# Kernel tuning notes

Measured on AMD Instinct MI355X. Metric: run time of the kernel, lower is better.

Reference implementation:

```python
import jax, jax.numpy as jnp
import numpy as np

MAX_AGENTS = 5
AGENT_DIM = 64
NUM_ACTIONS = 10
BATCH = 131072


def setup_inputs() -> dict:
    key = jax.random.key(0)
    ks = jax.random.split(key, 20)
    def lin(k, out_d, in_d):
        kw, kb = jax.random.split(k)
        W = jax.random.normal(kw, (out_d, in_d), jnp.float32) * (1.0 / np.sqrt(in_d))
        b = jax.random.normal(kb, (out_d,), jnp.float32) * 0.02
        return W, b
    x = jax.random.normal(ks[0], (BATCH, MAX_AGENTS * AGENT_DIM), jnp.float32)
    Wk, bk = lin(ks[1], 32, AGENT_DIM)
    Wq, bq = lin(ks[2], 32, AGENT_DIM)
    Wv, bv = lin(ks[3], 64, AGENT_DIM)
    Wr, br = lin(ks[4], 32, 32)
    Wp1, bp1 = lin(ks[5], 64, 64)
    Wp2, bp2 = lin(ks[6], MAX_AGENTS * NUM_ACTIONS, 64)
    Wh1, bh1 = lin(ks[7], 64, 64)
    Wh2, bh2 = lin(ks[8], 1, 64)
    return {"x": x, "Wk": Wk, "bk": bk, "Wq": Wq, "bq": bq, "Wv": Wv, "bv": bv,
            "Wr": Wr, "br": br, "Wp1": Wp1, "bp1": bp1, "Wp2": Wp2, "bp2": bp2,
            "Wh1": Wh1, "bh1": bh1, "Wh2": Wh2, "bh2": bh2}


def reference(x, Wk, bk, Wq, bq, Wv, bv, Wr, br, Wp1, bp1, Wp2, bp2, Wh1, bh1, Wh2, bh2):
    B = x.shape[0]
    agents = x.reshape(B, MAX_AGENTS, AGENT_DIM)  # [B, A, D]
    keys = agents @ Wk.T + bk      # [B, A, 32]
    queries = agents @ Wq.T + bq   # [B, A, 32]
    values = agents @ Wv.T + bv    # [B, A, 64]
    scale = 1.0 / np.sqrt(32.0)
    attn = jnp.einsum('bqd,bkd->bqk', queries, keys) * scale
    rq = queries @ Wr.T + br       # [B, A, 32]
    attn = attn + jnp.einsum('bqd,bkd->bqk', rq, rq) * scale
    attn = jax.nn.softmax(attn, axis=-1)
    context = jnp.einsum('bqk,bkd->bqd', attn, values)  # [B, A, 64]
    agent_mask = (jnp.abs(agents).sum(axis=-1, keepdims=True) > 0.01).astype(x.dtype)  # [B, A, 1]
    pooled = (context * agent_mask).sum(axis=1) / (agent_mask.sum(axis=1) + 1e-8)  # [B, 64]
    h = jax.nn.gelu(pooled @ Wp1.T + bp1, approximate=False)
    action_logits = (h @ Wp2.T + bp2).reshape(B, MAX_AGENTS, NUM_ACTIONS)
    hv = jax.nn.gelu(pooled @ Wh1.T + bh1, approximate=False)
    value = hv @ Wh2.T + bh2  # [B, 1]
    return action_logits, value
```

## Files before the change

kernel.cpp:

```cpp
#include <hip/hip_runtime.h>
#include <stdint.h>


typedef __attribute__((ext_vector_type(8))) short bf16x8;
typedef __attribute__((ext_vector_type(4))) float f32x4;

#define ESTR 168
#define HSTR 136

#define WF1_OFF 0
#define BC_OFF  40960
#define WF2_OFF 41600
#define WF3_OFF 57984
#define BMLP_OFF 74368
#define BCOMB_OFF 74880
#define WRP_OFF 75136

__device__ __forceinline__ float b2f_lo(unsigned int pk) {
  union { unsigned int i; float f; } v; v.i = pk << 16; return v.f;
}
__device__ __forceinline__ float b2f_hi(unsigned int pk) {
  union { unsigned int i; float f; } v; v.i = pk & 0xffff0000u; return v.f;
}
__device__ __forceinline__ float b2f(unsigned short u) {
  union { unsigned int i; float f; } v; v.i = ((unsigned int)u) << 16; return v.f;
}
__device__ __forceinline__ unsigned short f2b(float f) {
  union { float f; unsigned int i; } v; v.f = f;
  unsigned int u = v.i;
  return (unsigned short)((u + 0x7fffu + ((u >> 16) & 1u)) >> 16);
}

__global__ void setup_a(const float* __restrict__ Wr,
                        const float* __restrict__ Wq,
                        char* __restrict__ ws) {
  int id = blockIdx.x * 256 + threadIdx.x;
  if (id >= 32 * 64) return;
  int rr = id >> 6, d = id & 63;
  float acc = 0.f;
#pragma unroll 8
  for (int m = 0; m < 32; ++m) acc += Wr[rr * 32 + m] * Wq[m * 64 + d];
  ((float*)(ws + WRP_OFF))[id] = acc;
}

__global__ void setup_b(const float* __restrict__ Wk,
                        const float* __restrict__ bk,
                        const float* __restrict__ Wq,
                        const float* __restrict__ bq,
                        const float* __restrict__ Wv,
                        const float* __restrict__ bv,
                        const float* __restrict__ Wr,
                        const float* __restrict__ br,
                        const float* __restrict__ Wp1,
                        const float* __restrict__ bp1,
                        const float* __restrict__ Wh1,
                        const float* __restrict__ bh1,
                        const float* __restrict__ Wp2,
                        const float* __restrict__ bp2,
                        const float* __restrict__ Wh2,
                        const float* __restrict__ bh2,
                        char* __restrict__ ws) {
  const float* Wrp = (const float*)(ws + WRP_OFF);
  unsigned short* wf1 = (unsigned short*)(ws + WF1_OFF);
  float* bc = (float*)(ws + BC_OFF);
  unsigned short* wf2 = (unsigned short*)(ws + WF2_OFF);
  unsigned short* wf3 = (unsigned short*)(ws + WF3_OFF);
  float* bmlp = (float*)(ws + BMLP_OFF);
  float* bcomb = (float*)(ws + BCOMB_OFF);

  int gid = blockIdx.x * 256 + threadIdx.x;
  if (gid < 20480) {
    int i = gid;
    int j = i & 7, l = (i >> 3) & 63, f = i >> 9;
    int n = f >> 2, h = (f >> 1) & 1, s = f & 1;
    int r = n * 16 + (l & 15);
    int k = s * 32 + ((l >> 4) & 3) * 8 + j;
    float w;
    if (r < 32)      w = Wq[r * 64 + k];
    else if (r < 64) w = Wk[(r - 32) * 64 + k];
    else if (r < 96) w = Wrp[(r - 64) * 64 + k];
    else             w = Wv[(r - 96) * 64 + k];
    unsigned short hi = f2b(w);
    wf1[i] = h ? f2b(w - b2f(hi)) : hi;
  } else if (gid < 28672) {
    int i = gid - 20480;
    int j = i & 7, l = (i >> 3) & 63, fs = i >> 9;
    int nt = fs >> 1, s = fs & 1;
    int n = nt * 16 + (l & 15);
    int k = s * 32 + ((l >> 4) & 3) * 8 + j;
    float wv = (n < 64) ? Wp1[n * 64 + k] : Wh1[(n - 64) * 64 + k];
    wf2[i] = f2b(wv);
  } else if (gid < 36864) {
    int i = gid - 28672;
    int j = i & 7, l = (i >> 3) & 63, f = i >> 9;
    int nt = f >> 2, s = f & 3;
    int o = nt * 16 + (l & 15);
    int k = s * 32 + ((l >> 4) & 3) * 8 + j;
    float wv = 0.f;
    if (o < 50 && k < 64)        wv = Wp2[o * 64 + k];
    else if (o == 50 && k >= 64) wv = Wh2[k - 64];
    wf3[i] = f2b(wv);
  } else {
    int sid = gid - 36864;
    if (sid < 160) {
      int r = sid;
      float v;
      if (r < 32)      v = bq[r];
      else if (r < 64) v = bk[r - 32];
      else if (r < 96) {
        int rr = r - 64;
        float acc = br[rr];
        for (int m = 0; m < 32; ++m) acc += Wr[rr * 32 + m] * bq[m];
        v = acc;
      } else            v = bv[r - 96];
      bc[r] = v;
    } else if (sid < 288) {
      int c = sid - 160;
      bmlp[c] = (c < 64) ? bp1[c] : bh1[c - 64];
    } else if (sid < 352) {
      int o = sid - 288;
      bcomb[o] = (o < 50) ? bp2[o] : ((o == 50) ? bh2[0] : 0.f);
    }
  }
}

__global__ __launch_bounds__(512, 2)
void policy_kernel(const float* __restrict__ x,
                   const char* __restrict__ ws,
                   float* __restrict__ out, int B) {
  __shared__ __align__(16) char shpool[74880];
  unsigned short* Els = (unsigned short*)shpool;
  float* maskLs = (float*)(shpool + 53760);
  unsigned short* xfrag = (unsigned short*)(shpool + 54400);
  float* asw  = (float*)(shpool + 54400);
  float* wkLs = (float*)(shpool + 57600);
  float* invLs = (float*)(shpool + 58240);
  unsigned short* pHi = (unsigned short*)(shpool + 58368);
  unsigned short* pLo = (unsigned short*)(shpool + 62464);
  unsigned short* HHi = (unsigned short*)shpool;
  unsigned short* HLo = (unsigned short*)(shpool + 8704);

  const int t = threadIdx.x;
  const int w = t >> 6, lane = t & 63;
  const int l15 = lane & 15, quad = lane >> 4;

  const uint4* wf1 = (const uint4*)(ws + WF1_OFF);
  const float* bc = (const float*)(ws + BC_OFF);
  const uint4* wf2 = (const uint4*)(ws + WF2_OFF);
  const uint4* wf3 = (const uint4*)(ws + WF3_OFF);
  const float* bmlp = (const float*)(ws + BMLP_OFF);
  const float* bcomb = (const float*)(ws + BCOMB_OFF);

  for (int m = w; m < 10; m += 8) {
    long row = (long)blockIdx.x * 160 + m * 16 + l15;
    const float* xr = x + row * 64 + quad * 8;
    float xv[16];
    *(float4*)(xv + 0)  = *(const float4*)(xr);
    *(float4*)(xv + 4)  = *(const float4*)(xr + 4);
    *(float4*)(xv + 8)  = *(const float4*)(xr + 32);
    *(float4*)(xv + 12) = *(const float4*)(xr + 36);
    float ms = 0.f;
#pragma unroll
    for (int i = 0; i < 16; ++i) ms += fabsf(xv[i]);
    ms += __shfl_xor(ms, 16, 64);
    ms += __shfl_xor(ms, 32, 64);
    if (quad == 0) maskLs[m * 16 + l15] = (ms > 0.01f) ? 1.f : 0.f;
    unsigned int pk[8];
#pragma unroll
    for (int i = 0; i < 8; ++i)
      pk[i] = (unsigned int)f2b(xv[2 * i]) |
              ((unsigned int)f2b(xv[2 * i + 1]) << 16);
    *(uint4*)&xfrag[((m * 2 + 0) * 64 + lane) * 8] =
        make_uint4(pk[0], pk[1], pk[2], pk[3]);
    *(uint4*)&xfrag[((m * 2 + 1) * 64 + lane) * 8] =
        make_uint4(pk[4], pk[5], pk[6], pk[7]);
  }
  __syncthreads();

  {
    union { uint4 u; bf16x8 v; } ah0, ah1, al0, al1, b0, b1;
    int ncur = -1;
    float4 bb = {0.f, 0.f, 0.f, 0.f};
    const int start = (w < 4) ? w * 13 : 52 + (w - 4) * 12;
    const int cnt = (w < 4) ? 13 : 12;
    for (int ti = 0; ti < cnt; ++ti) {
      int tt = start + ti;
      int n = tt / 10, m = tt - n * 10;
      if (n != ncur) {
        ncur = n;
        ah0.u = wf1[(n * 4 + 0) * 64 + lane];
        ah1.u = wf1[(n * 4 + 1) * 64 + lane];
        al0.u = wf1[(n * 4 + 2) * 64 + lane];
        al1.u = wf1[(n * 4 + 3) * 64 + lane];
        bb = *(const float4*)&bc[n * 16 + quad * 4];
      }
      b0.u = *(const uint4*)&xfrag[((m * 2 + 0) * 64 + lane) * 8];
      b1.u = *(const uint4*)&xfrag[((m * 2 + 1) * 64 + lane) * 8];
      f32x4 acc = {bb.x, bb.y, bb.z, bb.w};
      acc = __builtin_amdgcn_mfma_f32_16x16x32_bf16(ah0.v, b0.v, acc, 0, 0, 0);
      acc = __builtin_amdgcn_mfma_f32_16x16x32_bf16(ah1.v, b1.v, acc, 0, 0, 0);
      acc = __builtin_amdgcn_mfma_f32_16x16x32_bf16(al0.v, b0.v, acc, 0, 0, 0);
      acc = __builtin_amdgcn_mfma_f32_16x16x32_bf16(al1.v, b1.v, acc, 0, 0, 0);
      unsigned int u0 = (unsigned int)f2b(acc[0]) |
                        ((unsigned int)f2b(acc[1]) << 16);
      unsigned int u1 = (unsigned int)f2b(acc[2]) |
                        ((unsigned int)f2b(acc[3]) << 16);
      *(uint2*)&Els[(m * 16 + l15) * ESTR + n * 16 + quad * 4] =
          make_uint2(u0, u1);
    }
  }
  __syncthreads();

  for (int ti = w; ti < 11; ti += 8) {
    const unsigned short* ra = &Els[(ti * 15 + l15) * ESTR];
    union { uint4 u; bf16x8 v; } a0, a1, b0;
    a0.u = *(const uint4*)&ra[quad * 8];
    b0.u = *(const uint4*)&ra[32 + quad * 8];
    a1.u = *(const uint4*)&ra[64 + quad * 8];
    f32x4 acc = {0.f, 0.f, 0.f, 0.f};
    acc = __builtin_amdgcn_mfma_f32_16x16x32_bf16(a0.v, b0.v, acc, 0, 0, 0);
    acc = __builtin_amdgcn_mfma_f32_16x16x32_bf16(a1.v, a1.v, acc, 0, 0, 0);
#pragma unroll
    for (int r = 0; r < 4; ++r) {
      int arq = ti * 15 + quad * 4 + r;
      int ark = ti * 15 + l15;
      int bq = arq / 5, qq = arq - 5 * bq;
      int bk2 = ark / 5, kk = ark - 5 * bk2;
      if (bq == bk2 && bq < 32)
        asw[bq * 25 + qq * 5 + kk] = acc[r] * 0.17677669529663689f;
    }
  }
  __syncthreads();

  if (t < 160) {
    const int b = t / 5, k = t - 5 * b;
    const float* ab = &asw[b * 25];
    float wk = 0.f;
#pragma unroll
    for (int q = 0; q < 5; ++q) {
      float s0 = ab[q * 5 + 0], s1 = ab[q * 5 + 1], s2 = ab[q * 5 + 2],
            s3 = ab[q * 5 + 3], s4 = ab[q * 5 + 4];
      float mx = fmaxf(fmaxf(fmaxf(s0, s1), fmaxf(s2, s3)), s4);
      float ps = __expf(s0 - mx) + __expf(s1 - mx) + __expf(s2 - mx) +
                 __expf(s3 - mx) + __expf(s4 - mx);
      float ek = __expf(ab[q * 5 + k] - mx);
      wk += maskLs[b * 5 + q] * __fdividef(ek, ps);
    }
    wkLs[t] = wk;
  }
  if (t < 32) {
    float msum = maskLs[t * 5] + maskLs[t * 5 + 1] + maskLs[t * 5 + 2] +
                 maskLs[t * 5 + 3] + maskLs[t * 5 + 4];
    invLs[t] = 1.0f / (msum + 1e-8f);
  }
  __syncthreads();

  for (int i = t; i < 32 * 32; i += 512) {
    int b = i >> 5, d0 = (i & 31) * 2;
    const float* wk = &wkLs[b * 5];
    float a0 = 0.f, a1 = 0.f;
#pragma unroll
    for (int k = 0; k < 5; ++k) {
      unsigned int v = *(const unsigned int*)&Els[(5 * b + k) * ESTR + 96 + d0];
      a0 = __builtin_fmaf(wk[k], b2f_lo(v), a0);
      a1 = __builtin_fmaf(wk[k], b2f_hi(v), a1);
    }
    float inv = invLs[b];
    float p0 = a0 * inv, p1 = a1 * inv;
    unsigned short h0 = f2b(p0), h1 = f2b(p1);
    unsigned short l0 = f2b(p0 - b2f(h0)), l1 = f2b(p1 - b2f(h1));
    int fi = (((b >> 4) * 2 + (d0 >> 5)) * 64 + ((d0 >> 3) & 3) * 16 + (b & 15))
                 * 8 + (d0 & 7);
    *(unsigned int*)&pHi[fi] = (unsigned int)h0 | ((unsigned int)h1 << 16);
    *(unsigned int*)&pLo[fi] = (unsigned int)l0 | ((unsigned int)l1 << 16);
  }
  __syncthreads();

  {
    const int mt = w >> 2;
    union { uint4 u; bf16x8 v; } pH0, pH1, pL0, pL1;
    pH0.u = *(const uint4*)&pHi[((mt * 2 + 0) * 64 + lane) * 8];
    pH1.u = *(const uint4*)&pHi[((mt * 2 + 1) * 64 + lane) * 8];
    pL0.u = *(const uint4*)&pLo[((mt * 2 + 0) * 64 + lane) * 8];
    pL1.u = *(const uint4*)&pLo[((mt * 2 + 1) * 64 + lane) * 8];
#pragma unroll
    for (int tI = 0; tI < 2; ++tI) {
      int cht = (w & 3) * 2 + tI;
      union { uint4 u; bf16x8 v; } aw0, aw1;
      aw0.u = wf2[(cht * 2 + 0) * 64 + lane];
      aw1.u = wf2[(cht * 2 + 1) * 64 + lane];
      float4 bb = *(const float4*)&bmlp[cht * 16 + quad * 4];
      f32x4 acc = {bb.x, bb.y, bb.z, bb.w};
      acc = __builtin_amdgcn_mfma_f32_16x16x32_bf16(aw0.v, pH0.v, acc, 0, 0, 0);
      acc = __builtin_amdgcn_mfma_f32_16x16x32_bf16(aw1.v, pH1.v, acc, 0, 0, 0);
      acc = __builtin_amdgcn_mfma_f32_16x16x32_bf16(aw0.v, pL0.v, acc, 0, 0, 0);
      acc = __builtin_amdgcn_mfma_f32_16x16x32_bf16(aw1.v, pL1.v, acc, 0, 0, 0);
      unsigned short hi[4], lo[4];
#pragma unroll
      for (int r = 0; r < 4; ++r) {
        float v = acc[r];
        float g = 0.5f * v * (1.0f + erff(v * 0.70710678118654752f));
        hi[r] = f2b(g);
        lo[r] = f2b(g - b2f(hi[r]));
      }
      int base = (mt * 16 + l15) * HSTR + cht * 16 + quad * 4;
      *(uint2*)&HHi[base] = make_uint2(
          (unsigned int)hi[0] | ((unsigned int)hi[1] << 16),
          (unsigned int)hi[2] | ((unsigned int)hi[3] << 16));
      *(uint2*)&HLo[base] = make_uint2(
          (unsigned int)lo[0] | ((unsigned int)lo[1] << 16),
          (unsigned int)lo[2] | ((unsigned int)lo[3] << 16));
    }
  }
  __syncthreads();

  {
    const int mt = w >> 2, nt = w & 3;
    const int row = mt * 16 + l15;
    union { uint4 u; bf16x8 v; } a[4], bh[4], bl[4];
#pragma unroll
    for (int s = 0; s < 4; ++s) {
      a[s].u = wf3[(nt * 4 + s) * 64 + lane];
      bh[s].u = *(const uint4*)&HHi[row * HSTR + s * 32 + quad * 8];
      bl[s].u = *(const uint4*)&HLo[row * HSTR + s * 32 + quad * 8];
    }
    float4 bb = *(const float4*)&bcomb[nt * 16 + quad * 4];
    f32x4 acc = {bb.x, bb.y, bb.z, bb.w};
#pragma unroll
    for (int s = 0; s < 4; ++s) {
      acc = __builtin_amdgcn_mfma_f32_16x16x32_bf16(a[s].v, bh[s].v, acc, 0, 0, 0);
      acc = __builtin_amdgcn_mfma_f32_16x16x32_bf16(a[s].v, bl[s].v, acc, 0, 0, 0);
    }
    long gb = (long)blockIdx.x * 32 + row;
    int o0 = nt * 16 + quad * 4;
#pragma unroll
    for (int r = 0; r < 4; ++r) {
      int o = o0 + r;
      if (o < 50)       out[gb * 50 + o] = acc[r];
      else if (o == 50) out[(long)B * 50 + gb] = acc[r];
    }
  }
}

extern "C" void kernel_launch(void* const* d_in, const int* in_sizes, int n_in,
                              void* d_out, int out_size, void* d_ws, size_t ws_size,
                              hipStream_t stream) {
  const float* x   = (const float*)d_in[0];
  const float* Wk  = (const float*)d_in[1];
  const float* bk  = (const float*)d_in[2];
  const float* Wq  = (const float*)d_in[3];
  const float* bq  = (const float*)d_in[4];
  const float* Wv  = (const float*)d_in[5];
  const float* bv  = (const float*)d_in[6];
  const float* Wr  = (const float*)d_in[7];
  const float* br  = (const float*)d_in[8];
  const float* Wp1 = (const float*)d_in[9];
  const float* bp1 = (const float*)d_in[10];
  const float* Wp2 = (const float*)d_in[11];
  const float* bp2 = (const float*)d_in[12];
  const float* Wh1 = (const float*)d_in[13];
  const float* bh1 = (const float*)d_in[14];
  const float* Wh2 = (const float*)d_in[15];
  const float* bh2 = (const float*)d_in[16];

  int B = in_sizes[0] / 320;

  setup_a<<<8, 256, 0, stream>>>(Wr, Wq, (char*)d_ws);
  setup_b<<<145, 256, 0, stream>>>(Wk, bk, Wq, bq, Wv, bv, Wr, br,
                                   Wp1, bp1, Wh1, bh1, Wp2, bp2, Wh2, bh2,
                                   (char*)d_ws);
  policy_kernel<<<B / 32, 512, 0, stream>>>(x, (const char*)d_ws,
                                            (float*)d_out, B);
}
```

Before: 313.9 us.

## Fold query/key/relation weights into one bilinear form and fold Wv into the MLP

Precomputes G = (Wq^T Wk + Wrq^T Wrq)·scale so attention scores become x·G·x^T. This replaces separate Q, K, RQ and V projections with a single 64x64 projection per agent followed by a dot with raw x. The value projection is folded into the first MLP layers (Wp1·Wv, Wh1·Wv plus a mask-weighted bias vector), so pooling runs on raw x. The last layer gets a hi/lo split of the weights for accuracy. The aim is fewer MFMAs and less shared memory, which may improve occupancy, at the cost of more setup work and different rounding.

```diff
diff --git a/kernel.cpp b/kernel.cpp
--- a/kernel.cpp
+++ b/kernel.cpp
@@ -5,16 +5,17 @@
 typedef __attribute__((ext_vector_type(8))) short bf16x8;
 typedef __attribute__((ext_vector_type(4))) float f32x4;
 
-#define ESTR 168
 #define HSTR 136
-
-#define WF1_OFF 0
-#define BC_OFF  40960
-#define WF2_OFF 41600
-#define WF3_OFF 57984
-#define BMLP_OFF 74368
-#define BCOMB_OFF 74880
-#define WRP_OFF 75136
+#define SCALE 0.17677669529663689f
+
+#define WRQ_OFF 0
+#define WF1_OFF 8192
+#define BCG_OFF 24576
+#define WF2_OFF 24832
+#define UV_OFF  41216
+#define WF3_OFF 41728
+#define BMLP_OFF 74496
+#define BCOMB_OFF 75008
 
 __device__ __forceinline__ float b2f_lo(unsigned int pk) {
   union { unsigned int i; float f; } v; v.i = pk << 16; return v.f;
@@ -29,6 +30,12 @@
   union { float f; unsigned int i; } v; v.f = f;
   unsigned int u = v.i;
   return (unsigned short)((u + 0x7fffu + ((u >> 16) & 1u)) >> 16);
+}
+__device__ __forceinline__ unsigned int pack2(float a, float b) {
+  return (unsigned int)f2b(a) | ((unsigned int)f2b(b) << 16);
+}
+__device__ __forceinline__ float gelu_e(float v) {
+  return 0.5f * v * (1.0f + erff(v * 0.70710678118654752f));
 }
 
 __global__ void setup_a(const float* __restrict__ Wr,
@@ -40,7 +47,7 @@
   float acc = 0.f;
 #pragma unroll 8
   for (int m = 0; m < 32; ++m) acc += Wr[rr * 32 + m] * Wq[m * 64 + d];
-  ((float*)(ws + WRP_OFF))[id] = acc;
+  ((float*)(ws + WRQ_OFF))[id] = acc;
 }
 
 __global__ void setup_b(const float* __restrict__ Wk,
@@ -60,67 +67,75 @@
                         const float* __restrict__ Wh2,
                         const float* __restrict__ bh2,
                         char* __restrict__ ws) {
-  const float* Wrp = (const float*)(ws + WRP_OFF);
+  const float* Wrq = (const float*)(ws + WRQ_OFF);
   unsigned short* wf1 = (unsigned short*)(ws + WF1_OFF);
-  float* bc = (float*)(ws + BC_OFF);
+  float* bcG = (float*)(ws + BCG_OFF);
   unsigned short* wf2 = (unsigned short*)(ws + WF2_OFF);
+  float* uvec = (float*)(ws + UV_OFF);
   unsigned short* wf3 = (unsigned short*)(ws + WF3_OFF);
   float* bmlp = (float*)(ws + BMLP_OFF);
   float* bcomb = (float*)(ws + BCOMB_OFF);
 
   int gid = blockIdx.x * 256 + threadIdx.x;
-  if (gid < 20480) {
+  if (gid < 8192) {
     int i = gid;
     int j = i & 7, l = (i >> 3) & 63, f = i >> 9;
     int n = f >> 2, h = (f >> 1) & 1, s = f & 1;
-    int r = n * 16 + (l & 15);
-    int k = s * 32 + ((l >> 4) & 3) * 8 + j;
-    float w;
-    if (r < 32)      w = Wq[r * 64 + k];
-    else if (r < 64) w = Wk[(r - 32) * 64 + k];
-    else if (r < 96) w = Wrp[(r - 64) * 64 + k];
-    else             w = Wv[(r - 96) * 64 + k];
-    unsigned short hi = f2b(w);
-    wf1[i] = h ? f2b(w - b2f(hi)) : hi;
-  } else if (gid < 28672) {
-    int i = gid - 20480;
-    int j = i & 7, l = (i >> 3) & 63, fs = i >> 9;
-    int nt = fs >> 1, s = fs & 1;
-    int n = nt * 16 + (l & 15);
-    int k = s * 32 + ((l >> 4) & 3) * 8 + j;
-    float wv = (n < 64) ? Wp1[n * 64 + k] : Wh1[(n - 64) * 64 + k];
-    wf2[i] = f2b(wv);
-  } else if (gid < 36864) {
-    int i = gid - 28672;
+    int d = n * 16 + (l & 15);
+    int e = s * 32 + ((l >> 4) & 3) * 8 + j;
+    float acc = 0.f;
+    for (int m = 0; m < 32; ++m)
+      acc += Wq[m * 64 + e] * Wk[m * 64 + d] +
+             Wrq[m * 64 + e] * Wrq[m * 64 + d];
+    float wv = acc * SCALE;
+    unsigned short hi = f2b(wv);
+    wf1[i] = h ? f2b(wv - b2f(hi)) : hi;
+  } else if (gid < 8256) {
+    int d = gid - 8192;
+    float acc = 0.f;
+    for (int m = 0; m < 32; ++m) {
+      float brr = br[m];
+      for (int j2 = 0; j2 < 32; ++j2) brr += Wr[m * 32 + j2] * bq[j2];
+      acc += Wk[m * 64 + d] * bq[m] + Wrq[m * 64 + d] * brr;
+    }
+    bcG[d] = acc * SCALE;
+  } else if (gid < 16448) {
+    int i = gid - 8256;
     int j = i & 7, l = (i >> 3) & 63, f = i >> 9;
-    int nt = f >> 2, s = f & 3;
+    int cht = f >> 1, s = f & 1;
+    int c = cht * 16 + (l & 15);
+    int e = s * 32 + ((l >> 4) & 3) * 8 + j;
+    float acc = 0.f;
+    for (int d = 0; d < 64; ++d) {
+      float wm = (c < 64) ? Wp1[c * 64 + d] : Wh1[(c - 64) * 64 + d];
+      acc += wm * Wv[d * 64 + e];
+    }
+    wf2[i] = f2b(acc);
+  } else if (gid < 16576) {
+    int c = gid - 16448;
+    float acc = 0.f;
+    for (int d = 0; d < 64; ++d) {
+      float wm = (c < 64) ? Wp1[c * 64 + d] : Wh1[(c - 64) * 64 + d];
+      acc += wm * bv[d];
+    }
+    uvec[c] = acc;
+  } else if (gid < 32960) {
+    int i = gid - 16576;
+    int j = i & 7, l = (i >> 3) & 63, f = i >> 9;
+    int nt = f >> 3, s = (f >> 1) & 3, h = f & 1;
     int o = nt * 16 + (l & 15);
     int k = s * 32 + ((l >> 4) & 3) * 8 + j;
     float wv = 0.f;
     if (o < 50 && k < 64)        wv = Wp2[o * 64 + k];
     else if (o == 50 && k >= 64) wv = Wh2[k - 64];
-    wf3[i] = f2b(wv);
-  } else {
-    int sid = gid - 36864;
-    if (sid < 160) {
-      int r = sid;
-      float v;
-      if (r < 32)      v = bq[r];
-      else if (r < 64) v = bk[r - 32];
-      else if (r < 96) {
-        int rr = r - 64;
-        float acc = br[rr];
-        for (int m = 0; m < 32; ++m) acc += Wr[rr * 32 + m] * bq[m];
-        v = acc;
-      } else            v = bv[r - 96];
-      bc[r] = v;
-    } else if (sid < 288) {
-      int c = sid - 160;
-      bmlp[c] = (c < 64) ? bp1[c] : bh1[c - 64];
-    } else if (sid < 352) {
-      int o = sid - 288;
-      bcomb[o] = (o < 50) ? bp2[o] : ((o == 50) ? bh2[0] : 0.f);
-    }
+    unsigned short hi = f2b(wv);
+    wf3[i] = h ? f2b(wv - b2f(hi)) : hi;
+  } else if (gid < 33088) {
+    int c = gid - 32960;
+    bmlp[c] = (c < 64) ? bp1[c] : bh1[c - 64];
+  } else if (gid < 33152) {
+    int o = gid - 33088;
+    bcomb[o] = (o < 50) ? bp2[o] : ((o == 50) ? bh2[0] : 0.f);
   }
 }
 
@@ -128,28 +143,22 @@
 void policy_kernel(const float* __restrict__ x,
                    const char* __restrict__ ws,
                    float* __restrict__ out, int B) {
-  __shared__ __align__(16) char shpool[74880];
-  unsigned short* Els = (unsigned short*)shpool;
-  float* maskLs = (float*)(shpool + 53760);
-  unsigned short* xfrag = (unsigned short*)(shpool + 54400);
-  float* asw  = (float*)(shpool + 54400);
-  float* wkLs = (float*)(shpool + 57600);
-  float* invLs = (float*)(shpool + 58240);
-  unsigned short* pHi = (unsigned short*)(shpool + 58368);
-  unsigned short* pLo = (unsigned short*)(shpool + 62464);
-  unsigned short* HHi = (unsigned short*)shpool;
-  unsigned short* HLo = (unsigned short*)(shpool + 8704);
+  __shared__ __align__(16) char shpool[50688];
+  unsigned short* xfrag = (unsigned short*)shpool;
+  unsigned short* gfrag = (unsigned short*)(shpool + 20480);
+  float* maskLs = (float*)(shpool + 40960);
+  float* asw = (float*)(shpool + 41600);
+  unsigned short* pXHi = (unsigned short*)(shpool + 41600);
+  unsigned short* pXLo = (unsigned short*)(shpool + 45696);
+  float* wkLs  = (float*)(shpool + 49792);
+  float* invLs = (float*)(shpool + 50432);
+  float* skLs  = (float*)(shpool + 50560);
+  unsigned short* HHi = (unsigned short*)(shpool + 20480);
+  unsigned short* HLo = (unsigned short*)(shpool + 29184);
 
   const int t = threadIdx.x;
   const int w = t >> 6, lane = t & 63;
   const int l15 = lane & 15, quad = lane >> 4;
-
-  const uint4* wf1 = (const uint4*)(ws + WF1_OFF);
-  const float* bc = (const float*)(ws + BC_OFF);
-  const uint4* wf2 = (const uint4*)(ws + WF2_OFF);
-  const uint4* wf3 = (const uint4*)(ws + WF3_OFF);
-  const float* bmlp = (const float*)(ws + BMLP_OFF);
-  const float* bcomb = (const float*)(ws + BCOMB_OFF);
 
   for (int m = w; m < 10; m += 8) {
     long row = (long)blockIdx.x * 160 + m * 16 + l15;
@@ -167,9 +176,7 @@
     if (quad == 0) maskLs[m * 16 + l15] = (ms > 0.01f) ? 1.f : 0.f;
     unsigned int pk[8];
 #pragma unroll
-    for (int i = 0; i < 8; ++i)
-      pk[i] = (unsigned int)f2b(xv[2 * i]) |
-              ((unsigned int)f2b(xv[2 * i + 1]) << 16);
+    for (int i = 0; i < 8; ++i) pk[i] = pack2(xv[2 * i], xv[2 * i + 1]);
     *(uint4*)&xfrag[((m * 2 + 0) * 64 + lane) * 8] =
         make_uint4(pk[0], pk[1], pk[2], pk[3]);
     *(uint4*)&xfrag[((m * 2 + 1) * 64 + lane) * 8] =
@@ -178,56 +185,54 @@
   __syncthreads();
 
   {
-    union { uint4 u; bf16x8 v; } ah0, ah1, al0, al1, b0, b1;
-    int ncur = -1;
-    float4 bb = {0.f, 0.f, 0.f, 0.f};
-    const int start = (w < 4) ? w * 13 : 52 + (w - 4) * 12;
-    const int cnt = (w < 4) ? 13 : 12;
-    for (int ti = 0; ti < cnt; ++ti) {
-      int tt = start + ti;
-      int n = tt / 10, m = tt - n * 10;
-      if (n != ncur) {
-        ncur = n;
-        ah0.u = wf1[(n * 4 + 0) * 64 + lane];
-        ah1.u = wf1[(n * 4 + 1) * 64 + lane];
-        al0.u = wf1[(n * 4 + 2) * 64 + lane];
-        al1.u = wf1[(n * 4 + 3) * 64 + lane];
-        bb = *(const float4*)&bc[n * 16 + quad * 4];
-      }
+    const int n = w >> 1;
+    const uint4* wf1 = (const uint4*)(ws + WF1_OFF);
+    const float* bcG = (const float*)(ws + BCG_OFF);
+    union { uint4 u; bf16x8 v; } wh0, wh1, wl0, wl1, b0, b1;
+    wh0.u = wf1[(n * 4 + 0) * 64 + lane];
+    wh1.u = wf1[(n * 4 + 1) * 64 + lane];
+    wl0.u = wf1[(n * 4 + 2) * 64 + lane];
+    wl1.u = wf1[(n * 4 + 3) * 64 + lane];
+    float4 bb = *(const float4*)&bcG[n * 16 + quad * 4];
+    const int c0 = n * 16 + quad * 4;
+    const int gb0 = ((c0 >> 5) * 64 + ((c0 >> 3) & 3) * 16 + l15) * 8 + (c0 & 7);
+#pragma unroll
+    for (int mi = 0; mi < 5; ++mi) {
+      int m = (w & 1) * 5 + mi;
       b0.u = *(const uint4*)&xfrag[((m * 2 + 0) * 64 + lane) * 8];
       b1.u = *(const uint4*)&xfrag[((m * 2 + 1) * 64 + lane) * 8];
       f32x4 acc = {bb.x, bb.y, bb.z, bb.w};
-      acc = __builtin_amdgcn_mfma_f32_16x16x32_bf16(ah0.v, b0.v, acc, 0, 0, 0);
-      acc = __builtin_amdgcn_mfma_f32_16x16x32_bf16(ah1.v, b1.v, acc, 0, 0, 0);
-      acc = __builtin_amdgcn_mfma_f32_16x16x32_bf16(al0.v, b0.v, acc, 0, 0, 0);
-      acc = __builtin_amdgcn_mfma_f32_16x16x32_bf16(al1.v, b1.v, acc, 0, 0, 0);
-      unsigned int u0 = (unsigned int)f2b(acc[0]) |
-                        ((unsigned int)f2b(acc[1]) << 16);
-      unsigned int u1 = (unsigned int)f2b(acc[2]) |
-                        ((unsigned int)f2b(acc[3]) << 16);
-      *(uint2*)&Els[(m * 16 + l15) * ESTR + n * 16 + quad * 4] =
-          make_uint2(u0, u1);
+      acc = __builtin_amdgcn_mfma_f32_16x16x32_bf16(wh0.v, b0.v, acc, 0, 0, 0);
+      acc = __builtin_amdgcn_mfma_f32_16x16x32_bf16(wh1.v, b1.v, acc, 0, 0, 0);
+      acc = __builtin_amdgcn_mfma_f32_16x16x32_bf16(wl0.v, b0.v, acc, 0, 0, 0);
+      acc = __builtin_amdgcn_mfma_f32_16x16x32_bf16(wl1.v, b1.v, acc, 0, 0, 0);
+      *(uint2*)&gfrag[m * 1024 + gb0] =
+          make_uint2(pack2(acc[0], acc[1]), pack2(acc[2], acc[3]));
     }
   }
   __syncthreads();
 
   for (int ti = w; ti < 11; ti += 8) {
-    const unsigned short* ra = &Els[(ti * 15 + l15) * ESTR];
-    union { uint4 u; bf16x8 v; } a0, a1, b0;
-    a0.u = *(const uint4*)&ra[quad * 8];
-    b0.u = *(const uint4*)&ra[32 + quad * 8];
-    a1.u = *(const uint4*)&ra[64 + quad * 8];
+    int r = ti * 15 + l15;
+    if (r > 159) r = 159;
+    int fo = (r >> 4) * 1024 + quad * 128 + (r & 15) * 8;
+    union { uint4 u; bf16x8 v; } a0, a1, b0, b1;
+    a0.u = *(const uint4*)&gfrag[fo];
+    a1.u = *(const uint4*)&gfrag[fo + 512];
+    b0.u = *(const uint4*)&xfrag[fo];
+    b1.u = *(const uint4*)&xfrag[fo + 512];
     f32x4 acc = {0.f, 0.f, 0.f, 0.f};
     acc = __builtin_amdgcn_mfma_f32_16x16x32_bf16(a0.v, b0.v, acc, 0, 0, 0);
-    acc = __builtin_amdgcn_mfma_f32_16x16x32_bf16(a1.v, a1.v, acc, 0, 0, 0);
-#pragma unroll
-    for (int r = 0; r < 4; ++r) {
-      int arq = ti * 15 + quad * 4 + r;
-      int ark = ti * 15 + l15;
-      int bq = arq / 5, qq = arq - 5 * bq;
-      int bk2 = ark / 5, kk = ark - 5 * bk2;
-      if (bq == bk2 && bq < 32)
-        asw[bq * 25 + qq * 5 + kk] = acc[r] * 0.17677669529663689f;
+    acc = __builtin_amdgcn_mfma_f32_16x16x32_bf16(a1.v, b1.v, acc, 0, 0, 0);
+    int wbk = (13 * l15) >> 6, kk = l15 - 5 * wbk;
+    bool kval = (l15 < 15);
+#pragma unroll
+    for (int rr = 0; rr < 4; ++rr) {
+      int lr = quad * 4 + rr;
+      int wb = (13 * lr) >> 6, qq = lr - 5 * wb;
+      int b = ti * 3 + wb;
+      if (lr < 15 && kval && wb == wbk && b < 32)
+        asw[b * 25 + qq * 5 + kk] = acc[rr];
     }
   }
   __syncthreads();
@@ -251,7 +256,9 @@
   if (t < 32) {
     float msum = maskLs[t * 5] + maskLs[t * 5 + 1] + maskLs[t * 5 + 2] +
                  maskLs[t * 5 + 3] + maskLs[t * 5 + 4];
-    invLs[t] = 1.0f / (msum + 1e-8f);
+    float inv = 1.0f / (msum + 1e-8f);
+    invLs[t] = inv;
+    skLs[t] = msum * inv;
   }
   __syncthreads();
 
@@ -261,36 +268,46 @@
     float a0 = 0.f, a1 = 0.f;
 #pragma unroll
     for (int k = 0; k < 5; ++k) {
-      unsigned int v = *(const unsigned int*)&Els[(5 * b + k) * ESTR + 96 + d0];
+      int rr = 5 * b + k;
+      int ad = ((rr >> 4) * 2 + (d0 >> 5)) * 512 + ((d0 >> 3) & 3) * 128 +
+               (rr & 15) * 8 + (d0 & 7);
+      unsigned int v = *(const unsigned int*)&xfrag[ad];
       a0 = __builtin_fmaf(wk[k], b2f_lo(v), a0);
       a1 = __builtin_fmaf(wk[k], b2f_hi(v), a1);
     }
     float inv = invLs[b];
     float p0 = a0 * inv, p1 = a1 * inv;
     unsigned short h0 = f2b(p0), h1 = f2b(p1);
-    unsigned short l0 = f2b(p0 - b2f(h0)), l1 = f2b(p1 - b2f(h1));
+    float r0 = p0 - b2f(h0), r1 = p1 - b2f(h1);
     int fi = (((b >> 4) * 2 + (d0 >> 5)) * 64 + ((d0 >> 3) & 3) * 16 + (b & 15))
                  * 8 + (d0 & 7);
-    *(unsigned int*)&pHi[fi] = (unsigned int)h0 | ((unsigned int)h1 << 16);
-    *(unsigned int*)&pLo[fi] = (unsigned int)l0 | ((unsigned int)l1 << 16);
+    *(unsigned int*)&pXHi[fi] = (unsigned int)h0 | ((unsigned int)h1 << 16);
+    *(unsigned int*)&pXLo[fi] = pack2(r0, r1);
   }
   __syncthreads();
 
   {
     const int mt = w >> 2;
-    union { uint4 u; bf16x8 v; } pH0, pH1, pL0, pL1;
-    pH0.u = *(const uint4*)&pHi[((mt * 2 + 0) * 64 + lane) * 8];
-    pH1.u = *(const uint4*)&pHi[((mt * 2 + 1) * 64 + lane) * 8];
-    pL0.u = *(const uint4*)&pLo[((mt * 2 + 0) * 64 + lane) * 8];
-    pL1.u = *(const uint4*)&pLo[((mt * 2 + 1) * 64 + lane) * 8];
+    const uint4* wf2 = (const uint4*)(ws + WF2_OFF);
+    const float* bmlp = (const float*)(ws + BMLP_OFF);
+    const float* uvec = (const float*)(ws + UV_OFF);
+    union { uint4 u; bf16x8 v; } pH0, pH1, pL0, pL1, aw0, aw1;
+    pH0.u = *(const uint4*)&pXHi[((mt * 2 + 0) * 64 + lane) * 8];
+    pH1.u = *(const uint4*)&pXHi[((mt * 2 + 1) * 64 + lane) * 8];
+    pL0.u = *(const uint4*)&pXLo[((mt * 2 + 0) * 64 + lane) * 8];
+    pL1.u = *(const uint4*)&pXLo[((mt * 2 + 1) * 64 + lane) * 8];
+    float skb = skLs[mt * 16 + l15];
 #pragma unroll
     for (int tI = 0; tI < 2; ++tI) {
       int cht = (w & 3) * 2 + tI;
-      union { uint4 u; bf16x8 v; } aw0, aw1;
       aw0.u = wf2[(cht * 2 + 0) * 64 + lane];
       aw1.u = wf2[(cht * 2 + 1) * 64 + lane];
-      float4 bb = *(const float4*)&bmlp[cht * 16 + quad * 4];
-      f32x4 acc = {bb.x, bb.y, bb.z, bb.w};
+      float4 bm = *(const float4*)&bmlp[cht * 16 + quad * 4];
+      float4 uu = *(const float4*)&uvec[cht * 16 + quad * 4];
+      f32x4 acc = {__builtin_fmaf(skb, uu.x, bm.x),
+                   __builtin_fmaf(skb, uu.y, bm.y),
+                   __builtin_fmaf(skb, uu.z, bm.z),
+                   __builtin_fmaf(skb, uu.w, bm.w)};
       acc = __builtin_amdgcn_mfma_f32_16x16x32_bf16(aw0.v, pH0.v, acc, 0, 0, 0);
       acc = __builtin_amdgcn_mfma_f32_16x16x32_bf16(aw1.v, pH1.v, acc, 0, 0, 0);
       acc = __builtin_amdgcn_mfma_f32_16x16x32_bf16(aw0.v, pL0.v, acc, 0, 0, 0);
@@ -298,8 +315,7 @@
       unsigned short hi[4], lo[4];
 #pragma unroll
       for (int r = 0; r < 4; ++r) {
-        float v = acc[r];
-        float g = 0.5f * v * (1.0f + erff(v * 0.70710678118654752f));
+        float g = gelu_e(acc[r]);
         hi[r] = f2b(g);
         lo[r] = f2b(g - b2f(hi[r]));
       }
@@ -317,27 +333,28 @@
   {
     const int mt = w >> 2, nt = w & 3;
     const int row = mt * 16 + l15;
-    union { uint4 u; bf16x8 v; } a[4], bh[4], bl[4];
-#pragma unroll
-    for (int s = 0; s < 4; ++s) {
-      a[s].u = wf3[(nt * 4 + s) * 64 + lane];
-      bh[s].u = *(const uint4*)&HHi[row * HSTR + s * 32 + quad * 8];
-      bl[s].u = *(const uint4*)&HLo[row * HSTR + s * 32 + quad * 8];
-    }
+    const uint4* wf3 = (const uint4*)(ws + WF3_OFF);
+    const float* bcomb = (const float*)(ws + BCOMB_OFF);
     float4 bb = *(const float4*)&bcomb[nt * 16 + quad * 4];
     f32x4 acc = {bb.x, bb.y, bb.z, bb.w};
+    union { uint4 u; bf16x8 v; } ah, al, bh, bl;
 #pragma unroll
     for (int s = 0; s < 4; ++s) {
-      acc = __builtin_amdgcn_mfma_f32_16x16x32_bf16(a[s].v, bh[s].v, acc, 0, 0, 0);
-      acc = __builtin_amdgcn_mfma_f32_16x16x32_bf16(a[s].v, bl[s].v, acc, 0, 0, 0);
+      ah.u = wf3[(nt * 8 + s * 2 + 0) * 64 + lane];
+      al.u = wf3[(nt * 8 + s * 2 + 1) * 64 + lane];
+      bh.u = *(const uint4*)&HHi[row * HSTR + s * 32 + quad * 8];
+      bl.u = *(const uint4*)&HLo[row * HSTR + s * 32 + quad * 8];
+      acc = __builtin_amdgcn_mfma_f32_16x16x32_bf16(ah.v, bh.v, acc, 0, 0, 0);
+      acc = __builtin_amdgcn_mfma_f32_16x16x32_bf16(ah.v, bl.v, acc, 0, 0, 0);
+      acc = __builtin_amdgcn_mfma_f32_16x16x32_bf16(al.v, bh.v, acc, 0, 0, 0);
     }
     long gb = (long)blockIdx.x * 32 + row;
     int o0 = nt * 16 + quad * 4;
 #pragma unroll
-    for (int r = 0; r < 4; ++r) {
-      int o = o0 + r;
-      if (o < 50)       out[gb * 50 + o] = acc[r];
-      else if (o == 50) out[(long)B * 50 + gb] = acc[r];
+    for (int rr = 0; rr < 4; ++rr) {
+      int o = o0 + rr;
+      if (o < 50)       out[gb * 50 + o] = acc[rr];
+      else if (o == 50) out[(long)B * 50 + gb] = acc[rr];
     }
   }
 }
@@ -366,7 +383,7 @@
   int B = in_sizes[0] / 320;
 
   setup_a<<<8, 256, 0, stream>>>(Wr, Wq, (char*)d_ws);
-  setup_b<<<145, 256, 0, stream>>>(Wk, bk, Wq, bq, Wv, bv, Wr, br,
+  setup_b<<<130, 256, 0, stream>>>(Wk, bk, Wq, bq, Wv, bv, Wr, br,
                                    Wp1, bp1, Wh1, bh1, Wp2, bp2, Wh2, bh2,
                                    (char*)d_ws);
   policy_kernel<<<B / 32, 512, 0, stream>>>(x, (const char*)d_ws,
```

Measured after the change: 299.9 us. 1.05x faster.
